# Kernel optimization log

Measured on AMD Instinct MI355X. Metric: run time of the kernel, lower is better.

## Reference

```python
import jax, jax.numpy as jnp
import numpy as np

EPS = 1e-5
NUM_HEADS = 4
TEMP = 0.1


def setup_inputs() -> dict:
    key = jax.random.key(0)
    ks = jax.random.split(key, 12)
    n, c, s, p, k = 64, 256, 64, 16, 4
    sc = 1.0 / np.sqrt(c)
    return {
        "x": jax.random.normal(ks[0], (n, c, s, p), dtype=jnp.float32),
        "prototypes": jax.random.normal(ks[1], (p, k, c), dtype=jnp.float32),
        "Wq": jax.random.normal(ks[2], (c, c), dtype=jnp.float32) * sc,
        "bq": jnp.zeros((c,), dtype=jnp.float32),
        "Wk": jax.random.normal(ks[3], (c, c), dtype=jnp.float32) * sc,
        "bk": jnp.zeros((c,), dtype=jnp.float32),
        "Wv": jax.random.normal(ks[4], (c, c), dtype=jnp.float32) * sc,
        "bv": jnp.zeros((c,), dtype=jnp.float32),
        "Wo": jax.random.normal(ks[5], (c, c), dtype=jnp.float32) * sc,
        "bo": jnp.zeros((c,), dtype=jnp.float32),
        "fc_bin": jax.random.normal(ks[6], (p, k * c, c), dtype=jnp.float32) * (1.0 / np.sqrt(k * c)),
    }


def _causal_attention(x, Wq, bq, Wk, bk, Wv, bv, Wo, bo):
    # x: (B, S, C) -> multi-head causal self-attention
    B, S, C = x.shape
    H = NUM_HEADS
    D = C // H
    q = (x @ Wq + bq).reshape(B, S, H, D).transpose(0, 2, 1, 3)
    k = (x @ Wk + bk).reshape(B, S, H, D).transpose(0, 2, 1, 3)
    v = (x @ Wv + bv).reshape(B, S, H, D).transpose(0, 2, 1, 3)
    scores = jnp.einsum('bhqd,bhkd->bhqk', q, k) / jnp.sqrt(jnp.float32(D))
    causal = jnp.tril(jnp.ones((S, S), dtype=bool))
    scores = jnp.where(causal, scores, jnp.finfo(scores.dtype).min)
    attn = jax.nn.softmax(scores, axis=-1)
    out = jnp.einsum('bhqk,bhkd->bhqd', attn, v)
    out = out.transpose(0, 2, 1, 3).reshape(B, S, C)
    return out @ Wo + bo


def reference(x, prototypes, Wq, bq, Wk, bk, Wv, bv, Wo, bo, fc_bin):
    n, c, s, p = x.shape
    kclusters = prototypes.shape[1]
    # n c s p -> p n s c
    x_part = x.transpose(3, 0, 2, 1)
    # InstanceNorm1d over the temporal (s) axis per (p, n, c)
    mu = x_part.mean(axis=2, keepdims=True)
    var = x_part.var(axis=2, keepdims=True)
    x_normed = (x_part - mu) / jnp.sqrt(var + EPS)
    # cosine similarity with prototypes
    xn = x_normed / jnp.linalg.norm(x_normed, axis=-1, keepdims=True)
    pn = prototypes / jnp.linalg.norm(prototypes, axis=-1, keepdims=True)
    sim = jnp.einsum('pnsc,pkc->pnsk', xn, pn)
    # straight-through hard/soft assignment (training=True path)
    soft = jax.nn.softmax(sim / TEMP, axis=-1)
    hard_idx = jnp.argmax(soft, axis=-1)                      # (p, n, s)
    hard = jax.nn.one_hot(hard_idx, kclusters, dtype=soft.dtype)
    assignment = jax.lax.stop_gradient(hard - soft) + soft    # (p, n, s, k)
    # mode over parts -> per-(n, s) cluster index
    idx_nsp = hard_idx.transpose(1, 2, 0)                     # (n, s, p)
    counts = jax.nn.one_hot(idx_nsp, kclusters, dtype=jnp.float32).sum(axis=2)
    cluster_indices = jnp.argmax(counts, axis=-1)             # (n, s)
    # causal attention with residual, batched over (n p)
    x2 = x.transpose(0, 3, 2, 1).reshape(n * p, s, c)         # (n p) s c
    x_attn = _causal_attention(x2, Wq, bq, Wk, bk, Wv, bv, Wo, bo) + x2
    x_attn = x_attn.reshape(n, p, s, c).transpose(1, 0, 2, 3)  # p n s c
    # scatter-max pooling: assignment-weighted max over time per cluster
    asg = assignment.transpose(0, 1, 3, 2)[..., None]         # (p, n, k, s, 1)
    grouped = asg * x_attn[:, :, None, :, :]                  # (p, n, k, s, c)
    clustered = grouped.max(axis=3)                           # (p, n, k, c)
    clustered = clustered.transpose(1, 2, 3, 0).reshape(n, kclusters * c, p)
    # SeparateFCs: per-part linear
    out = jnp.einsum('ncp,pco->nop', clustered, fc_bin)       # (n, c_out, p)
    return out, cluster_indices
```

## Files before the change

kernel.cpp:

```cpp
#include <hip/hip_runtime.h>

typedef unsigned short u16;
typedef unsigned int u32;
typedef __attribute__((ext_vector_type(8))) short bf16x8;
typedef __attribute__((ext_vector_type(4))) float f32x4;

typedef __attribute__((address_space(1))) const unsigned int gu32;
typedef __attribute__((address_space(3))) unsigned int lu32;

#define FMIN32 -3.402823466e38f

__device__ inline u16 f2bf(float f) {
    u32 x = __float_as_uint(f);
    u32 r = x + 0x7FFFu + ((x >> 16) & 1u);
    return (u16)(r >> 16);
}
__device__ inline float bf2f(u16 u) { return __uint_as_float(((u32)u) << 16); }

__device__ inline double wave_sum_d(double v) {
#pragma unroll
    for (int m = 1; m < 64; m <<= 1) v += __shfl_xor(v, m, 64);
    return v;
}

__global__ __launch_bounds__(256) void convert_w(const float* W0, const float* W1,
                                                 const float* W2, const float* W3, u16* Wt) {
    const float* Ws[4] = {W0, W1, W2, W3};
    int z = blockIdx.z;
    const float* W = Ws[z];
    u16* O = Wt + (size_t)z * 65536;
    __shared__ float tl[32][33];
    int t = threadIdx.x;
    int bx = blockIdx.x, by = blockIdx.y;
#pragma unroll
    for (int i = 0; i < 4; i++) {
        int e = i * 256 + t; int tr = e >> 5, tc = e & 31;
        tl[tr][tc] = W[(size_t)(bx * 32 + tr) * 256 + by * 32 + tc];
    }
    __syncthreads();
#pragma unroll
    for (int i = 0; i < 4; i++) {
        int e = i * 256 + t; int tr = e >> 5, tc = e & 31;
        O[(size_t)(by * 32 + tr) * 256 + bx * 32 + tc] = f2bf(tl[tc][tr]);
    }
}

__global__ __launch_bounds__(256) void convert_fc(const float* F, u16* O) {
    int p = blockIdx.z;
    int bx = blockIdx.x, by = blockIdx.y;
    const float* Fp = F + (size_t)p * 1024 * 256;
    u16* Op = O + (size_t)p * 256 * 1024;
    __shared__ float tl[32][33];
    int t = threadIdx.x;
#pragma unroll
    for (int i = 0; i < 4; i++) {
        int e = i * 256 + t; int tr = e >> 5, tc = e & 31;
        tl[tr][tc] = Fp[(size_t)(bx * 32 + tr) * 256 + by * 32 + tc];
    }
    __syncthreads();
#pragma unroll
    for (int i = 0; i < 4; i++) {
        int e = i * 256 + t; int tr = e >> 5, tc = e & 31;
        Op[(size_t)(by * 32 + tr) * 1024 + bx * 32 + tc] = f2bf(tl[tc][tr]);
    }
}

__global__ __launch_bounds__(256) void transpose_x(const float* x, float* xt, u16* xtbf) {
    int bx = blockIdx.x;
    int nn = bx >> 6, s = bx & 63;
    __shared__ float tile[16][257];
    int t = threadIdx.x;
    const float* xb = x + (size_t)nn * 262144 + (size_t)s * 16;
#pragma unroll
    for (int chunk = 0; chunk < 16; chunk++) {
        int e = chunk * 256 + t;
        int c = e >> 4, pp = e & 15;
        tile[pp][c] = xb[(size_t)c * 1024 + pp];
    }
    __syncthreads();
#pragma unroll
    for (int pp = 0; pp < 16; pp++) {
        float v = tile[pp][t];
        size_t o = ((size_t)(nn * 16 + pp) * 64 + s) * 256 + t;
        xt[o] = v;
        xtbf[o] = f2bf(v);
    }
}

__global__ __launch_bounds__(256) void norm_sim(const float* xt, const float* prot, int* hard) {
    int b = blockIdx.x;
    int pp = b & 15, nn = b >> 4;
    __shared__ float xs[64][257];
    __shared__ double wk[4][256];
    __shared__ double smu[256];
    __shared__ double srstd[256];
    __shared__ double offk[4];
    __shared__ double dd[64][5];
    int t = threadIdx.x, w = t >> 6, lane = t & 63;

    const float* xb = xt + (size_t)b * 64 * 256 + t;
    double s1 = 0.0, s2 = 0.0;
#pragma unroll 8
    for (int s = 0; s < 64; s++) {
        float v = xb[(size_t)s * 256];
        xs[s][t] = v;
        double dv = (double)v;
        s1 += dv; s2 += dv * dv;
    }
    double mu = s1 * (1.0 / 64.0);
    double var = s2 * (1.0 / 64.0) - mu * mu;
    smu[t] = mu;
    srstd[t] = 1.0 / sqrt(var + 1e-5);
    __syncthreads();

    {
        double pv[4]; double ss = 0.0;
#pragma unroll
        for (int j = 0; j < 4; j++) {
            pv[j] = (double)prot[((size_t)pp * 4 + w) * 256 + lane + 64 * j];
            ss += pv[j] * pv[j];
        }
        ss = wave_sum_d(ss);
        double rn = 1.0 / sqrt(ss);
        double po = 0.0;
#pragma unroll
        for (int j = 0; j < 4; j++) {
            int c = lane + 64 * j;
            double wv = pv[j] * rn * srstd[c];
            wk[w][c] = wv;
            po += wv * smu[c];
        }
        po = wave_sum_d(po);
        if (lane == 0) offk[w] = po;
    }
    __syncthreads();

    {
        int s = lane;
        const float* xr = &xs[s][0];
        const double* wr = &wk[w][0];
        double a0 = 0.0, a1 = 0.0, a2 = 0.0, a3 = 0.0;
#pragma unroll 8
        for (int c = 0; c < 256; c += 4) {
            a0 = fma((double)xr[c],     wr[c],     a0);
            a1 = fma((double)xr[c + 1], wr[c + 1], a1);
            a2 = fma((double)xr[c + 2], wr[c + 2], a2);
            a3 = fma((double)xr[c + 3], wr[c + 3], a3);
        }
        dd[s][w] = ((a0 + a1) + (a2 + a3)) - offk[w];
    }
    __syncthreads();

    if (t < 64) {
        double d0 = dd[t][0], d1 = dd[t][1], d2 = dd[t][2], d3 = dd[t][3];
        int best = 0; double bv = d0;
        if (d1 > bv) { bv = d1; best = 1; }
        if (d2 > bv) { bv = d2; best = 2; }
        if (d3 > bv) { best = 3; }
        hard[((pp * 64 + nn) << 6) + t] = best;
    }
}

__global__ __launch_bounds__(256) void cluster_mode(const int* hard, float* outp) {
    int tid = blockIdx.x * 256 + threadIdx.x;
    int nn = tid >> 6, s = tid & 63;
    int cnt[4] = {0, 0, 0, 0};
#pragma unroll
    for (int p = 0; p < 16; p++) cnt[hard[((p * 64 + nn) << 6) + s]]++;
    int best = 0;
#pragma unroll
    for (int k = 1; k < 4; k++) if (cnt[k] > cnt[best]) best = k;
    outp[tid] = (float)best;
}

__global__ __launch_bounds__(256) void fused_attn(const u16* xtbf, const u16* Wt,
                                                  const float* bq, const float* bk, const float* bv,
                                                  const float* bo, const int* hard, u16* clus) {
    __shared__ u16 xs[64][264];
    __shared__ u16 scr[4][64][72];
    __shared__ int sidx[64];
    int t = threadIdx.x;
    int w = t >> 6, lane = t & 63;
    int l15 = lane & 15, qd = lane >> 4;
    int b = blockIdx.x;
    int pp = b & 15, nn = b >> 4;

    {
        const u16* xb = xtbf + (size_t)b * 16384;
#pragma unroll
        for (int i = 0; i < 8; i++) {
            int e = i * 256 + t;
            int r = e >> 5, g = e & 31;
            *(uint4*)&xs[r][g * 8] = *(const uint4*)(xb + (size_t)r * 256 + g * 8);
        }
        if (t < 64) sidx[t] = hard[((pp * 64 + nn) << 6) + t];
    }
    __syncthreads();

    f32x4 acc[4][4];
    const f32x4 zero4 = {0.f, 0.f, 0.f, 0.f};

    auto gemm64 = [&](const u16* Wb) {
#pragma unroll
        for (int mt = 0; mt < 4; mt++)
#pragma unroll
            for (int nt = 0; nt < 4; nt++) acc[mt][nt] = zero4;
#pragma unroll
        for (int kc = 0; kc < 8; kc++) {
            bf16x8 af[4], bfr[4];
#pragma unroll
            for (int mt = 0; mt < 4; mt++)
                af[mt] = *(const bf16x8*)(&xs[mt * 16 + l15][kc * 32 + qd * 8]);
#pragma unroll
            for (int nt = 0; nt < 4; nt++)
                bfr[nt] = *(const bf16x8*)(Wb + (size_t)(nt * 16 + l15) * 256 + kc * 32 + qd * 8);
#pragma unroll
            for (int mt = 0; mt < 4; mt++)
#pragma unroll
                for (int nt = 0; nt < 4; nt++)
                    acc[mt][nt] = __builtin_amdgcn_mfma_f32_16x16x32_bf16(af[mt], bfr[nt], acc[mt][nt], 0, 0, 0);
        }
    };

    u16* sw = &scr[w][0][0];
    bf16x8 qf[2][4], kf[2][4];

    gemm64(Wt + (size_t)(w * 64) * 256);
#pragma unroll
    for (int mt = 0; mt < 4; mt++)
#pragma unroll
        for (int nt = 0; nt < 4; nt++) {
            int col = nt * 16 + l15;
            float bb = bq[w * 64 + col];
#pragma unroll
            for (int r = 0; r < 4; r++)
                sw[(mt * 16 + qd * 4 + r) * 72 + col] = f2bf(acc[mt][nt][r] + bb);
        }
#pragma unroll
    for (int kc2 = 0; kc2 < 2; kc2++)
#pragma unroll
        for (int mt = 0; mt < 4; mt++)
            qf[kc2][mt] = *(const bf16x8*)(sw + (mt * 16 + l15) * 72 + kc2 * 32 + qd * 8);

    gemm64(Wt + 65536 + (size_t)(w * 64) * 256);
#pragma unroll
    for (int mt = 0; mt < 4; mt++)
#pragma unroll
        for (int nt = 0; nt < 4; nt++) {
            int col = nt * 16 + l15;
            float bb = bk[w * 64 + col];
#pragma unroll
            for (int r = 0; r < 4; r++)
                sw[(mt * 16 + qd * 4 + r) * 72 + col] = f2bf(acc[mt][nt][r] + bb);
        }
#pragma unroll
    for (int kc2 = 0; kc2 < 2; kc2++)
#pragma unroll
        for (int mt = 0; mt < 4; mt++)
            kf[kc2][mt] = *(const bf16x8*)(sw + (mt * 16 + l15) * 72 + kc2 * 32 + qd * 8);

#pragma unroll
    for (int mt = 0; mt < 4; mt++)
#pragma unroll
        for (int nt = 0; nt < 4; nt++) acc[mt][nt] = zero4;
#pragma unroll
    for (int kc2 = 0; kc2 < 2; kc2++)
#pragma unroll
        for (int mt = 0; mt < 4; mt++)
#pragma unroll
            for (int nt = 0; nt < 4; nt++)
                acc[mt][nt] = __builtin_amdgcn_mfma_f32_16x16x32_bf16(qf[kc2][mt], kf[kc2][nt], acc[mt][nt], 0, 0, 0);

#pragma unroll
    for (int mt = 0; mt < 4; mt++) {
#pragma unroll
        for (int r = 0; r < 4; r++) {
            int row = mt * 16 + qd * 4 + r;
            float v[4];
#pragma unroll
            for (int nt = 0; nt < 4; nt++) {
                int col = nt * 16 + l15;
                float sv = acc[mt][nt][r] * 0.125f;
                if (col > row) sv = FMIN32;
                v[nt] = sv;
            }
            float m = fmaxf(fmaxf(v[0], v[1]), fmaxf(v[2], v[3]));
#pragma unroll
            for (int msk = 1; msk < 16; msk <<= 1) m = fmaxf(m, __shfl_xor(m, msk, 64));
            float e[4], ssum = 0.f;
#pragma unroll
            for (int nt = 0; nt < 4; nt++) { e[nt] = expf(v[nt] - m); ssum += e[nt]; }
#pragma unroll
            for (int msk = 1; msk < 16; msk <<= 1) ssum += __shfl_xor(ssum, msk, 64);
            float rinv = 1.0f / ssum;
#pragma unroll
            for (int nt = 0; nt < 4; nt++) sw[row * 72 + nt * 16 + l15] = f2bf(e[nt] * rinv);
        }
    }
    bf16x8 pf[2][4];
#pragma unroll
    for (int kc2 = 0; kc2 < 2; kc2++)
#pragma unroll
        for (int mt = 0; mt < 4; mt++)
            pf[kc2][mt] = *(const bf16x8*)(sw + (mt * 16 + l15) * 72 + kc2 * 32 + qd * 8);

    gemm64(Wt + 2 * 65536 + (size_t)(w * 64) * 256);
#pragma unroll
    for (int mt = 0; mt < 4; mt++)
#pragma unroll
        for (int nt = 0; nt < 4; nt++) {
            int d = nt * 16 + l15;
            float bb = bv[w * 64 + d];
            ushort4 pk;
            pk.x = f2bf(acc[mt][nt][0] + bb);
            pk.y = f2bf(acc[mt][nt][1] + bb);
            pk.z = f2bf(acc[mt][nt][2] + bb);
            pk.w = f2bf(acc[mt][nt][3] + bb);
            *(ushort4*)(sw + d * 72 + mt * 16 + qd * 4) = pk;
        }
    bf16x8 vf[2][4];
#pragma unroll
    for (int kc2 = 0; kc2 < 2; kc2++)
#pragma unroll
        for (int nt = 0; nt < 4; nt++)
            vf[kc2][nt] = *(const bf16x8*)(sw + (nt * 16 + l15) * 72 + kc2 * 32 + qd * 8);

#pragma unroll
    for (int mt = 0; mt < 4; mt++)
#pragma unroll
        for (int nt = 0; nt < 4; nt++) acc[mt][nt] = zero4;
#pragma unroll
    for (int kc2 = 0; kc2 < 2; kc2++)
#pragma unroll
        for (int nt = 0; nt < 4; nt++)
#pragma unroll
            for (int mt = 0; mt < 4; mt++)
                acc[mt][nt] = __builtin_amdgcn_mfma_f32_16x16x32_bf16(pf[kc2][mt], vf[kc2][nt], acc[mt][nt], 0, 0, 0);

#pragma unroll
    for (int mt = 0; mt < 4; mt++)
#pragma unroll
        for (int nt = 0; nt < 4; nt++)
#pragma unroll
            for (int r = 0; r < 4; r++)
                sw[(mt * 16 + qd * 4 + r) * 72 + nt * 16 + l15] = f2bf(acc[mt][nt][r]);
    __syncthreads();

    {
        const u16* WO = Wt + 3 * 65536 + (size_t)(w * 64) * 256;
#pragma unroll
        for (int mt = 0; mt < 4; mt++)
#pragma unroll
            for (int nt = 0; nt < 4; nt++) acc[mt][nt] = zero4;
#pragma unroll
        for (int kc = 0; kc < 8; kc++) {
            int h = kc >> 1, k2 = kc & 1;
            bf16x8 af[4], bfr[4];
#pragma unroll
            for (int mt = 0; mt < 4; mt++)
                af[mt] = *(const bf16x8*)(&scr[h][mt * 16 + l15][k2 * 32 + qd * 8]);
#pragma unroll
            for (int nt = 0; nt < 4; nt++)
                bfr[nt] = *(const bf16x8*)(WO + (size_t)(nt * 16 + l15) * 256 + kc * 32 + qd * 8);
#pragma unroll
            for (int mt = 0; mt < 4; mt++)
#pragma unroll
                for (int nt = 0; nt < 4; nt++)
                    acc[mt][nt] = __builtin_amdgcn_mfma_f32_16x16x32_bf16(af[mt], bfr[nt], acc[mt][nt], 0, 0, 0);
        }
    }

    int cnt[4] = {0, 0, 0, 0};
#pragma unroll
    for (int s = 0; s < 64; s++) cnt[sidx[s]]++;
    float ml[4][4];
#pragma unroll
    for (int nt = 0; nt < 4; nt++)
#pragma unroll
        for (int k = 0; k < 4; k++) ml[nt][k] = FMIN32;
#pragma unroll
    for (int mt = 0; mt < 4; mt++)
#pragma unroll
        for (int r = 0; r < 4; r++) {
            int s = mt * 16 + qd * 4 + r;
            int k = sidx[s];
#pragma unroll
            for (int nt = 0; nt < 4; nt++) {
                int col = w * 64 + nt * 16 + l15;
                float v = acc[mt][nt][r] + bo[col] + bf2f(xs[s][col]);
                ml[nt][k] = fmaxf(ml[nt][k], v);
            }
        }
#pragma unroll
    for (int nt = 0; nt < 4; nt++)
#pragma unroll
        for (int k = 0; k < 4; k++) {
            float m = ml[nt][k];
            m = fmaxf(m, __shfl_xor(m, 16, 64));
            m = fmaxf(m, __shfl_xor(m, 32, 64));
            if (cnt[k] < 64) m = fmaxf(m, 0.0f);
            ml[nt][k] = m;
        }
    if (qd == 0) {
        size_t ob = ((size_t)(pp * 64 + nn)) * 1024;
#pragma unroll
        for (int nt = 0; nt < 4; nt++) {
            int col = w * 64 + nt * 16 + l15;
#pragma unroll
            for (int k = 0; k < 4; k++)
                clus[ob + k * 256 + col] = f2bf(ml[nt][k]);
        }
    }
}

__global__ __launch_bounds__(256) void gemm_fc_mfma(const u16* clus, const u16* fcT, float* part) {
    int p = blockIdx.x, by = blockIdx.y, kz = blockIdx.z;
    __shared__ u16 As[64 * 32];
    __shared__ u16 Bs[64 * 32];
    const u16* Ap = clus + (size_t)p * 65536 + kz * 256;
    const u16* Bp = fcT + (size_t)p * 262144 + (size_t)(by * 64) * 1024 + kz * 256;
    int t = threadIdx.x;
    int w = t >> 6, lane = t & 63;
    int l15 = lane & 15, qd = lane >> 4;
    f32x4 acc[4] = {};
    int srow = t >> 2, scg = t & 3;
    for (int kc = 0; kc < 256; kc += 32) {
        *(uint4*)(As + srow * 32 + scg * 8) =
            *(const uint4*)(Ap + (size_t)srow * 1024 + kc + scg * 8);
        *(uint4*)(Bs + srow * 32 + scg * 8) =
            *(const uint4*)(Bp + (size_t)srow * 1024 + kc + scg * 8);
        __syncthreads();
        bf16x8 bfr = *(const bf16x8*)(Bs + (w * 16 + l15) * 32 + qd * 8);
#pragma unroll
        for (int mt = 0; mt < 4; mt++) {
            bf16x8 af = *(const bf16x8*)(As + (mt * 16 + l15) * 32 + qd * 8);
            acc[mt] = __builtin_amdgcn_mfma_f32_16x16x32_bf16(af, bfr, acc[mt], 0, 0, 0);
        }
        __syncthreads();
    }
#pragma unroll
    for (int mt = 0; mt < 4; mt++)
#pragma unroll
        for (int r = 0; r < 4; r++) {
            int n = mt * 16 + qd * 4 + r;
            int o = by * 64 + w * 16 + l15;
            part[(size_t)kz * 262144 + (size_t)n * 4096 + (size_t)o * 16 + p] = acc[mt][r];
        }
}

__global__ __launch_bounds__(256) void reduce_fc(const float* part, float* out) {
    int tid = blockIdx.x * 256 + threadIdx.x;
    const float4* p0 = (const float4*)part;
    float4 a = p0[tid];
    float4 b = p0[65536 + tid];
    float4 c = p0[131072 + tid];
    float4 d = p0[196608 + tid];
    float4 r;
    r.x = a.x + b.x + c.x + d.x;
    r.y = a.y + b.y + c.y + d.y;
    r.z = a.z + b.z + c.z + d.z;
    r.w = a.w + b.w + c.w + d.w;
    ((float4*)out)[tid] = r;
}

extern "C" void kernel_launch(void* const* d_in, const int* in_sizes, int n_in,
                              void* d_out, int out_size, void* d_ws, size_t ws_size,
                              hipStream_t stream) {
    const float* x    = (const float*)d_in[0];
    const float* prot = (const float*)d_in[1];
    const float* Wq   = (const float*)d_in[2];
    const float* bq   = (const float*)d_in[3];
    const float* Wk   = (const float*)d_in[4];
    const float* bk   = (const float*)d_in[5];
    const float* Wv   = (const float*)d_in[6];
    const float* bv   = (const float*)d_in[7];
    const float* Wo   = (const float*)d_in[8];
    const float* bo   = (const float*)d_in[9];
    const float* fcb  = (const float*)d_in[10];

    char* ws = (char*)d_ws;
    u16*   xtbf = (u16*)(ws + 0);
    float* xt   = (float*)(ws + 33554432);
    float* fcpart = (float*)(ws + 33554432);
    u16*   Wt   = (u16*)(ws + 134217728);
    u16*   fcT  = (u16*)(ws + 134742016);
    int*   hard = (int*)(ws + 143130624);
    u16*   clus = (u16*)(ws + 143392768);

    float* out_fc = (float*)d_out;
    float* out_ci = (float*)d_out + 262144;

    dim3 B(256);
    convert_w<<<dim3(8, 8, 4), B, 0, stream>>>(Wq, Wk, Wv, Wo, Wt);
    convert_fc<<<dim3(32, 8, 16), B, 0, stream>>>(fcb, fcT);
    transpose_x<<<dim3(4096), B, 0, stream>>>(x, xt, xtbf);
    norm_sim<<<dim3(1024), B, 0, stream>>>(xt, prot, hard);
    cluster_mode<<<dim3(16), B, 0, stream>>>(hard, out_ci);
    fused_attn<<<dim3(1024), B, 0, stream>>>(xtbf, Wt, bq, bk, bv, bo, hard, clus);
    gemm_fc_mfma<<<dim3(16, 4, 4), B, 0, stream>>>(clus, fcT, fcpart);
    reduce_fc<<<dim3(256), B, 0, stream>>>(fcpart, out_fc);
}
```

Baseline: 311.5 us.

## Drop LDS staging of x tile in fused attention; read A fragments from global

The fused attention kernel no longer copies the 64x256 bf16 x tile into shared memory. The QKV GEMM A-fragments and the residual add now read directly from global memory, relying on cache. The scatter-max epilogue is also restructured: the cluster counts come from a wave ballot/popcount, and the per-cluster max uses predicated selects instead of dynamically indexed register arrays. Dropping the roughly 33KB buffer and its barrier frees LDS for more occupancy, at the cost of repeated global/L2 reads of x across the three projections and four waves.

```diff
diff --git a/kernel.cpp b/kernel.cpp
--- a/kernel.cpp
+++ b/kernel.cpp
@@ -176,7 +176,6 @@
 __global__ __launch_bounds__(256) void fused_attn(const u16* xtbf, const u16* Wt,
                                                   const float* bq, const float* bk, const float* bv,
                                                   const float* bo, const int* hard, u16* clus) {
-    __shared__ u16 xs[64][264];
     __shared__ u16 scr[4][64][72];
     __shared__ int sidx[64];
     int t = threadIdx.x;
@@ -184,18 +183,9 @@
     int l15 = lane & 15, qd = lane >> 4;
     int b = blockIdx.x;
     int pp = b & 15, nn = b >> 4;
-
-    {
-        const u16* xb = xtbf + (size_t)b * 16384;
-#pragma unroll
-        for (int i = 0; i < 8; i++) {
-            int e = i * 256 + t;
-            int r = e >> 5, g = e & 31;
-            *(uint4*)&xs[r][g * 8] = *(const uint4*)(xb + (size_t)r * 256 + g * 8);
-        }
-        if (t < 64) sidx[t] = hard[((pp * 64 + nn) << 6) + t];
-    }
-    __syncthreads();
+    const u16* xb = xtbf + (size_t)b * 16384;
+
+    if (t < 64) sidx[t] = hard[((pp * 64 + nn) << 6) + t];
 
     f32x4 acc[4][4];
     const f32x4 zero4 = {0.f, 0.f, 0.f, 0.f};
@@ -210,7 +200,7 @@
             bf16x8 af[4], bfr[4];
 #pragma unroll
             for (int mt = 0; mt < 4; mt++)
-                af[mt] = *(const bf16x8*)(&xs[mt * 16 + l15][kc * 32 + qd * 8]);
+                af[mt] = *(const bf16x8*)(xb + (size_t)(mt * 16 + l15) * 256 + kc * 32 + qd * 8);
 #pragma unroll
             for (int nt = 0; nt < 4; nt++)
                 bfr[nt] = *(const bf16x8*)(Wb + (size_t)(nt * 16 + l15) * 256 + kc * 32 + qd * 8);
@@ -370,45 +360,48 @@
         }
     }
 
-    int cnt[4] = {0, 0, 0, 0};
-#pragma unroll
-    for (int s = 0; s < 64; s++) cnt[sidx[s]]++;
-    float ml[4][4];
-#pragma unroll
-    for (int nt = 0; nt < 4; nt++)
-#pragma unroll
-        for (int k = 0; k < 4; k++) ml[nt][k] = FMIN32;
-#pragma unroll
-    for (int mt = 0; mt < 4; mt++)
-#pragma unroll
-        for (int r = 0; r < 4; r++) {
-            int s = mt * 16 + qd * 4 + r;
-            int k = sidx[s];
-#pragma unroll
-            for (int nt = 0; nt < 4; nt++) {
-                int col = w * 64 + nt * 16 + l15;
-                float v = acc[mt][nt][r] + bo[col] + bf2f(xs[s][col]);
-                ml[nt][k] = fmaxf(ml[nt][k], v);
+#pragma unroll
+    for (int mt = 0; mt < 4; mt++)
+#pragma unroll
+        for (int nt = 0; nt < 4; nt++) {
+            int col = w * 64 + nt * 16 + l15;
+            float bb = bo[col];
+#pragma unroll
+            for (int r = 0; r < 4; r++) {
+                int s = mt * 16 + qd * 4 + r;
+                acc[mt][nt][r] += bb + bf2f(xb[(size_t)s * 256 + col]);
             }
         }
-#pragma unroll
-    for (int nt = 0; nt < 4; nt++)
-#pragma unroll
-        for (int k = 0; k < 4; k++) {
-            float m = ml[nt][k];
+    int myidx = sidx[lane];
+    int srow[16];
+#pragma unroll
+    for (int mt = 0; mt < 4; mt++)
+#pragma unroll
+        for (int r = 0; r < 4; r++) srow[mt * 4 + r] = sidx[mt * 16 + qd * 4 + r];
+    size_t ob = ((size_t)(pp * 64 + nn)) * 1024;
+#pragma unroll
+    for (int k = 0; k < 4; k++) {
+        unsigned long long bal = __ballot(myidx == k);
+        int ck = __popcll(bal);
+        float m0 = FMIN32, m1 = FMIN32, m2 = FMIN32, m3 = FMIN32;
+#pragma unroll
+        for (int mt = 0; mt < 4; mt++)
+#pragma unroll
+            for (int r = 0; r < 4; r++) {
+                bool tk = (srow[mt * 4 + r] == k);
+                m0 = tk ? fmaxf(m0, acc[mt][0][r]) : m0;
+                m1 = tk ? fmaxf(m1, acc[mt][1][r]) : m1;
+                m2 = tk ? fmaxf(m2, acc[mt][2][r]) : m2;
+                m3 = tk ? fmaxf(m3, acc[mt][3][r]) : m3;
+            }
+        float mm[4] = {m0, m1, m2, m3};
+#pragma unroll
+        for (int nt = 0; nt < 4; nt++) {
+            float m = mm[nt];
             m = fmaxf(m, __shfl_xor(m, 16, 64));
             m = fmaxf(m, __shfl_xor(m, 32, 64));
-            if (cnt[k] < 64) m = fmaxf(m, 0.0f);
-            ml[nt][k] = m;
-        }
-    if (qd == 0) {
-        size_t ob = ((size_t)(pp * 64 + nn)) * 1024;
-#pragma unroll
-        for (int nt = 0; nt < 4; nt++) {
-            int col = w * 64 + nt * 16 + l15;
-#pragma unroll
-            for (int k = 0; k < 4; k++)
-                clus[ob + k * 256 + col] = f2bf(ml[nt][k]);
+            if (ck < 64) m = fmaxf(m, 0.0f);
+            if (qd == 0) clus[ob + k * 256 + w * 64 + nt * 16 + l15] = f2bf(m);
         }
     }
 }
```

Measured after the change: 372.4 us. 19.5% more time.
